# Kernel optimization log

Hardware: AMD Instinct MI355X
Metric: run time of the kernel (lower is better)

Reference implementation:

```python
import jax, jax.numpy as jnp
import numpy as np
from jax import lax

GN_GROUPS = 8
GN_EPS = 1e-5
K_BITS = 8
DELTA = 0.05
EPS = 1e-8


def setup_inputs() -> dict:
    key = jax.random.key(0)
    k1, k2 = jax.random.split(key)
    B, Cin, H, W = 32, 256, 56, 56
    Cout, KS = 256, 3
    x = jax.random.normal(k1, (B, Cin, H, W), dtype=jnp.float32)
    # kaiming_normal_(nonlinearity='relu'): std = sqrt(2 / fan_in)
    fan_in = Cin * KS * KS
    weight_fp = jax.random.normal(k2, (Cout, Cin, KS, KS), dtype=jnp.float32) * np.sqrt(2.0 / fan_in)
    gamma = jnp.ones((Cin,), dtype=jnp.float32)
    beta = jnp.zeros((Cin,), dtype=jnp.float32)
    a = jnp.asarray(6.0, dtype=jnp.float32)  # PACT learnable clip
    bias = jnp.zeros((Cout,), dtype=jnp.float32)
    return {"x": x, "gamma": gamma, "beta": beta, "a": a, "weight_fp": weight_fp, "bias": bias}


def _group_norm(x, gamma, beta):
    B, C, H, W = x.shape
    xg = x.reshape(B, GN_GROUPS, -1)
    mu = xg.mean(axis=-1, keepdims=True)
    var = xg.var(axis=-1, keepdims=True)  # biased, matches torch GroupNorm
    xn = ((xg - mu) * lax.rsqrt(var + GN_EPS)).reshape(B, C, H, W)
    return xn * gamma[:, None, None] + beta[:, None, None]


def _pact_quant(x, a):
    a_c = jnp.maximum(a, 0.0) + EPS
    S = (2.0 ** K_BITS - 1.0) / a_c
    y = jnp.clip(x, 0.0, a_c)
    # straight-through round
    return y + lax.stop_gradient(jnp.round(y * S) / S - y)


def _ternary_weight(w_r):
    oc = w_r.shape[0]
    wv = w_r.reshape(oc, -1)
    wa = jnp.abs(wv)
    t = DELTA * wa.mean(axis=1, keepdims=True)
    m = (wa > t).astype(wv.dtype)
    alpha = (wa * m).sum(axis=1, keepdims=True) / (m.sum(axis=1, keepdims=True) + EPS)
    wq = (alpha * jnp.sign(wv) * m).reshape(w_r.shape)
    # STE gradient factor: m + 0.5*(1 - m)
    g = lax.stop_gradient((0.5 + 0.5 * m).reshape(w_r.shape))
    return g * w_r + lax.stop_gradient(wq - g * w_r)


def reference(x, gamma, beta, a, weight_fp, bias):
    h = _group_norm(x, gamma, beta)
    h = jnp.maximum(h, 0.0) ** 2          # ReLU^2
    h = _pact_quant(h, a)                  # PACT k-bit uniform quant
    w = _ternary_weight(weight_fp)         # ternary {-alpha, 0, +alpha}
    out = lax.conv_general_dilated(
        h, w, window_strides=(1, 1), padding=[(1, 1), (1, 1)],
        dimension_numbers=("NCHW", "OIHW", "NCHW"))
    return out + bias[:, None, None]
```

## Files before the change

### kernel.cpp

```cpp
#include <hip/hip_runtime.h>
#include <hip/hip_bf16.h>

#define B_    32
#define C_    256
#define H_    56
#define W_    56
#define HW_   3136
#define P_    58
#define G_    8
#define COUT_ 256
#define KTOT_ 2304

typedef float f32x4 __attribute__((ext_vector_type(4)));
typedef int   i32x4 __attribute__((ext_vector_type(4)));

__global__ __launch_bounds__(1024)
void gn_stats_kernel(const float* __restrict__ x, float* __restrict__ stats) {
    int bg = blockIdx.x;
    const float4* base = (const float4*)(x + (size_t)bg * (32 * HW_));
    float s1 = 0.f, s2 = 0.f;
    for (int i = threadIdx.x; i < 25088; i += 1024) {
        float4 v = base[i];
        s1 += v.x + v.y + v.z + v.w;
        s2 += v.x * v.x + v.y * v.y + v.z * v.z + v.w * v.w;
    }
    #pragma unroll
    for (int off = 32; off; off >>= 1) {
        s1 += __shfl_down(s1, off, 64);
        s2 += __shfl_down(s2, off, 64);
    }
    __shared__ float ra[16], rb[16];
    int lane = threadIdx.x & 63, wv = threadIdx.x >> 6;
    if (!lane) { ra[wv] = s1; rb[wv] = s2; }
    __syncthreads();
    if (threadIdx.x == 0) {
        float t1 = 0.f, t2 = 0.f;
        #pragma unroll
        for (int i = 0; i < 16; ++i) { t1 += ra[i]; t2 += rb[i]; }
        float mu = t1 / 100352.f;
        float var = t2 / 100352.f - mu * mu;
        stats[bg * 2]     = mu;
        stats[bg * 2 + 1] = rsqrtf(var + 1e-5f);
    }
}

__global__ __launch_bounds__(256)
void act_kernel(const float* __restrict__ x, const float* __restrict__ gamma,
                const float* __restrict__ beta, const float* __restrict__ a_ptr,
                const float* __restrict__ stats, char* __restrict__ q) {
    int by = blockIdx.x;
    int b = by / P_;
    int y = by - b * P_;
    char* qrow = q + (size_t)by * P_ * C_;
    const int PADV = 0x80808080;
    if (y == 0 || y == P_ - 1) {
        int4 pv = {PADV, PADV, PADV, PADV};
        for (int i = threadIdx.x; i < (P_ * C_) / 16; i += 256)
            ((int4*)qrow)[i] = pv;
        return;
    }
    int t = threadIdx.x;
    if (t < 64)            ((int*)qrow)[t] = PADV;
    else if (t < 128)      ((int*)(qrow + (P_ - 1) * C_))[t - 64] = PADV;

    float a_c = fmaxf(a_ptr[0], 0.f) + 1e-8f;
    float S   = 255.f / a_c;

    int c4 = t & 63;
    int wb = t >> 6;
    int g  = (4 * c4) >> 5;
    float mu = stats[(b * G_ + g) * 2];
    float rs = stats[(b * G_ + g) * 2 + 1];
    float ga[4], be[4];
    #pragma unroll
    for (int i = 0; i < 4; ++i) { ga[i] = gamma[4 * c4 + i]; be[i] = beta[4 * c4 + i]; }

    const float* xb = x + ((size_t)(b * C_ + 4 * c4)) * HW_ + (y - 1) * W_;
    for (int j = wb; j < 14; j += 4) {
        float4 v[4];
        #pragma unroll
        for (int i = 0; i < 4; ++i)
            v[i] = *(const float4*)(xb + (size_t)i * HW_ + j * 4);
        int qv[4][4];
        #pragma unroll
        for (int i = 0; i < 4; ++i) {
            float f[4] = {v[i].x, v[i].y, v[i].z, v[i].w};
            #pragma unroll
            for (int s = 0; s < 4; ++s) {
                float yv = (f[s] - mu) * rs * ga[i] + be[i];
                float r  = fmaxf(yv, 0.f);
                float h2 = fminf(r * r, a_c);
                qv[i][s] = (int)rintf(h2 * S) - 128;
            }
        }
        #pragma unroll
        for (int s = 0; s < 4; ++s) {
            int packed = (qv[0][s] & 255) | ((qv[1][s] & 255) << 8) |
                         ((qv[2][s] & 255) << 16) | (qv[3][s] << 24);
            *(int*)(qrow + (j * 4 + s + 1) * C_ + 4 * c4) = packed;
        }
    }
}

__global__ __launch_bounds__(256)
void wq_kernel(const float* __restrict__ wfp, char* __restrict__ wt,
               float* __restrict__ alphas, float* __restrict__ tsum) {
    int oc = blockIdx.x;
    int t  = threadIdx.x;
    const float* wr = wfp + (size_t)oc * KTOT_;
    float wl[9];
    float s = 0.f;
    #pragma unroll
    for (int j = 0; j < 9; ++j) { wl[j] = wr[t + j * 256]; s += fabsf(wl[j]); }

    __shared__ float red[4];
    int lane = t & 63, wv = t >> 6;
    #pragma unroll
    for (int off = 32; off; off >>= 1) s += __shfl_down(s, off, 64);
    if (!lane) red[wv] = s;
    __syncthreads();
    float thr = 0.05f * ((red[0] + red[1] + red[2] + red[3]) / (float)KTOT_);
    __syncthreads();

    float sm = 0.f, cnt = 0.f, ts = 0.f;
    #pragma unroll
    for (int j = 0; j < 9; ++j) {
        float aw = fabsf(wl[j]);
        if (aw > thr) {
            sm += aw; cnt += 1.f;
            ts += (wl[j] > 0.f) ? 1.f : -1.f;
        }
    }
    #pragma unroll
    for (int off = 32; off; off >>= 1) {
        sm  += __shfl_down(sm, off, 64);
        cnt += __shfl_down(cnt, off, 64);
        ts  += __shfl_down(ts, off, 64);
    }
    __shared__ float redc[4], redt[4];
    if (!lane) { red[wv] = sm; redc[wv] = cnt; redt[wv] = ts; }
    __syncthreads();
    if (t == 0) {
        float alpha = (red[0] + red[1] + red[2] + red[3]) /
                      (redc[0] + redc[1] + redc[2] + redc[3] + 1e-8f);
        alphas[oc] = alpha;
        tsum[oc] = redt[0] + redt[1] + redt[2] + redt[3];
    }
    #pragma unroll
    for (int j = 0; j < 9; ++j) {
        int i  = t + j * 256;
        int ic = i / 9;
        int tap = i - ic * 9;
        float w = wl[j];
        char tern = (fabsf(w) > thr) ? (w > 0.f ? (char)1 : (char)-1) : (char)0;
        wt[((size_t)tap * 256 + oc) * 256 + ic] = tern;
    }
}

__global__ __launch_bounds__(512)
void conv_gemm_kernel(const char* __restrict__ q, const char* __restrict__ wt,
                      const float* __restrict__ alphas, const float* __restrict__ bias,
                      const float* __restrict__ tsum, const float* __restrict__ a_ptr,
                      float* __restrict__ out) {
    int mt = blockIdx.x;
    int tid = threadIdx.x;
    int lane = tid & 63;
    int wv = tid >> 6;
    int wm = wv & 1, wn = wv >> 1;
    int quad = lane >> 4, lrow = lane & 15;

    __shared__ char As[128 * 128];
    __shared__ char Bs[256 * 128];

    int kswz = (((tid & 7) ^ ((tid >> 3) & 7)) << 4);
    int sb[2], wb[4];
    #pragma unroll
    for (int r = 0; r < 2; ++r) {
        int ml = r * 64 + (tid >> 3);
        int m = mt * 128 + ml;
        int b = m / HW_;
        int rem = m - b * HW_;
        int hh = rem / W_;
        int ww = rem - hh * W_;
        sb[r] = ((b * P_ + hh + 1) * P_ + (ww + 1)) * C_ + kswz;
    }
    #pragma unroll
    for (int r = 0; r < 4; ++r) {
        int oc = r * 64 + (tid >> 3);
        wb[r] = oc * C_ + kswz;
    }

    i32x4 acc[4][4];
    #pragma unroll
    for (int i = 0; i < 4; ++i)
        #pragma unroll
        for (int j = 0; j < 4; ++j) { acc[i][j][0]=0; acc[i][j][1]=0; acc[i][j][2]=0; acc[i][j][3]=0; }

    int arow = wm * 64 + lrow;
    int brow = wn * 64 + lrow;
    int rsw = lrow & 7;

    for (int kk = 0; kk < 18; ++kk) {
        int tap = kk >> 1;
        int ic0 = (kk & 1) << 7;
        int dh = tap / 3 - 1;
        int dw = tap - (tap / 3) * 3 - 1;
        int aoff = (dh * P_ + dw) * C_ + ic0;
        const char* gb = wt + (size_t)tap * (256 * 256) + ic0;
        #pragma unroll
        for (int r = 0; r < 2; ++r) {
            __builtin_amdgcn_global_load_lds(
                (const __attribute__((address_space(1))) void*)(q + sb[r] + aoff),
                (__attribute__((address_space(3))) void*)(&As[r * 8192 + tid * 16]),
                16, 0, 0);
        }
        #pragma unroll
        for (int r = 0; r < 4; ++r) {
            __builtin_amdgcn_global_load_lds(
                (const __attribute__((address_space(1))) void*)(gb + wb[r]),
                (__attribute__((address_space(3))) void*)(&Bs[r * 8192 + tid * 16]),
                16, 0, 0);
        }
        __syncthreads();
        #pragma unroll
        for (int ks = 0; ks < 2; ++ks) {
            int cb = (ks * 4 + quad) ^ rsw;
            i32x4 af[4], bf[4];
            #pragma unroll
            for (int mi = 0; mi < 4; ++mi)
                af[mi] = *(const i32x4*)&As[(arow + mi * 16) * 128 + cb * 16];
            #pragma unroll
            for (int ni = 0; ni < 4; ++ni)
                bf[ni] = *(const i32x4*)&Bs[(brow + ni * 16) * 128 + cb * 16];
            #pragma unroll
            for (int mi = 0; mi < 4; ++mi)
                #pragma unroll
                for (int ni = 0; ni < 4; ++ni)
                    acc[mi][ni] = __builtin_amdgcn_mfma_i32_16x16x64_i8(
                        af[mi], bf[ni], acc[mi][ni], 0, 0, 0);
        }
        __syncthreads();
    }

    float a_c = fmaxf(a_ptr[0], 0.f) + 1e-8f;
    float qs  = a_c * (1.f / 255.f);
    #pragma unroll
    for (int ni = 0; ni < 4; ++ni) {
        int n = wn * 64 + ni * 16 + lrow;
        float sc = alphas[n] * qs;
        float bn = bias[n];
        float corr = 128.f * tsum[n];
        #pragma unroll
        for (int mi = 0; mi < 4; ++mi) {
            int mbase = mt * 128 + wm * 64 + mi * 16 + quad * 4;
            int b = mbase / HW_;
            size_t off = (size_t)b * (C_ * HW_) + (size_t)n * HW_ + (mbase - b * HW_);
            f32x4 v;
            #pragma unroll
            for (int r = 0; r < 4; ++r)
                v[r] = ((float)acc[mi][ni][r] + corr) * sc + bn;
            *(f32x4*)(out + off) = v;
        }
    }
}

extern "C" void kernel_launch(void* const* d_in, const int* in_sizes, int n_in,
                              void* d_out, int out_size, void* d_ws, size_t ws_size,
                              hipStream_t stream) {
    const float* x     = (const float*)d_in[0];
    const float* gamma = (const float*)d_in[1];
    const float* beta  = (const float*)d_in[2];
    const float* a     = (const float*)d_in[3];
    const float* wfp   = (const float*)d_in[4];
    const float* bias  = (const float*)d_in[5];
    float* out = (float*)d_out;

    char* ws = (char*)d_ws;
    char*  qbuf   = ws;
    char*  wtb    = ws + 27557888;
    float* alphas = (float*)(ws + 27557888 + 589824);
    float* tsum   = alphas + 256;
    float* stats  = tsum + 256;

    gn_stats_kernel<<<B_ * G_, 1024, 0, stream>>>(x, stats);
    wq_kernel<<<COUT_, 256, 0, stream>>>(wfp, wtb, alphas, tsum);
    act_kernel<<<B_ * P_, 256, 0, stream>>>(x, gamma, beta, a, stats, qbuf);
    conv_gemm_kernel<<<784, 512, 0, stream>>>(qbuf, wtb, alphas, bias, tsum, a, out);
}
```

Before: 291.2 us.

## Double-buffer LDS tiles and interleave next-tile prefetch with MFMA phases

Splits shared memory into two buffers so the next K-step's A and B tiles are loaded asynchronously into LDS while the current tile is consumed. The MFMA work is broken into four phases separated by barriers, with the global-to-LDS loads spread between them, and s_setprio raises wave priority around the MFMA bursts. The goal is to hide global load latency behind compute. In exchange, LDS use doubles to 96KB per block, which may cut occupancy, and the extra barriers add synchronisation.

```diff
diff --git a/kernel.cpp b/kernel.cpp
--- a/kernel.cpp
+++ b/kernel.cpp
@@ -169,8 +169,8 @@
     int wm = wv & 1, wn = wv >> 1;
     int quad = lane >> 4, lrow = lane & 15;
 
-    __shared__ char As[128 * 128];
-    __shared__ char Bs[256 * 128];
+    __shared__ char As[2][128 * 128];
+    __shared__ char Bs[2][256 * 128];
 
     int kswz = (((tid & 7) ^ ((tid >> 3) & 7)) << 4);
     int sb[2], wb[4];
@@ -200,46 +200,114 @@
     int brow = wn * 64 + lrow;
     int rsw = lrow & 7;
 
-    for (int kk = 0; kk < 18; ++kk) {
+    auto stageA = [&](int kk, int buf) {
         int tap = kk >> 1;
         int ic0 = (kk & 1) << 7;
         int dh = tap / 3 - 1;
         int dw = tap - (tap / 3) * 3 - 1;
         int aoff = (dh * P_ + dw) * C_ + ic0;
-        const char* gb = wt + (size_t)tap * (256 * 256) + ic0;
         #pragma unroll
         for (int r = 0; r < 2; ++r) {
             __builtin_amdgcn_global_load_lds(
                 (const __attribute__((address_space(1))) void*)(q + sb[r] + aoff),
-                (__attribute__((address_space(3))) void*)(&As[r * 8192 + tid * 16]),
+                (__attribute__((address_space(3))) void*)(&As[buf][r * 8192 + tid * 16]),
                 16, 0, 0);
         }
-        #pragma unroll
-        for (int r = 0; r < 4; ++r) {
+    };
+    auto stageB = [&](int kk, int buf, int half) {
+        int tap = kk >> 1;
+        int ic0 = (kk & 1) << 7;
+        const char* gb = wt + (size_t)tap * (256 * 256) + ic0;
+        #pragma unroll
+        for (int r = 0; r < 2; ++r) {
+            int rr = half * 2 + r;
             __builtin_amdgcn_global_load_lds(
-                (const __attribute__((address_space(1))) void*)(gb + wb[r]),
-                (__attribute__((address_space(3))) void*)(&Bs[r * 8192 + tid * 16]),
+                (const __attribute__((address_space(1))) void*)(gb + wb[rr]),
+                (__attribute__((address_space(3))) void*)(&Bs[buf][rr * 8192 + tid * 16]),
                 16, 0, 0);
         }
+    };
+
+    stageA(0, 0);
+    stageB(0, 0, 0);
+    stageB(0, 0, 1);
+    __syncthreads();
+
+    int cur = 0;
+    for (int kk = 0; kk < 18; ++kk) {
+        int nxt = cur ^ 1;
+        bool pf = (kk < 17);
+        i32x4 bf[4];
+
+        if (pf) stageA(kk + 1, nxt);
+        {
+            int cb = quad ^ rsw;
+            #pragma unroll
+            for (int ni = 0; ni < 4; ++ni)
+                bf[ni] = *(const i32x4*)&Bs[cur][(brow + ni * 16) * 128 + cb * 16];
+            i32x4 a0 = *(const i32x4*)&As[cur][(arow +  0) * 128 + cb * 16];
+            i32x4 a1 = *(const i32x4*)&As[cur][(arow + 16) * 128 + cb * 16];
+            __builtin_amdgcn_s_setprio(1);
+            #pragma unroll
+            for (int ni = 0; ni < 4; ++ni)
+                acc[0][ni] = __builtin_amdgcn_mfma_i32_16x16x64_i8(a0, bf[ni], acc[0][ni], 0, 0, 0);
+            #pragma unroll
+            for (int ni = 0; ni < 4; ++ni)
+                acc[1][ni] = __builtin_amdgcn_mfma_i32_16x16x64_i8(a1, bf[ni], acc[1][ni], 0, 0, 0);
+            __builtin_amdgcn_s_setprio(0);
+        }
+        __builtin_amdgcn_s_barrier();
+
+        if (pf) stageB(kk + 1, nxt, 0);
+        {
+            int cb = quad ^ rsw;
+            i32x4 a2 = *(const i32x4*)&As[cur][(arow + 32) * 128 + cb * 16];
+            i32x4 a3 = *(const i32x4*)&As[cur][(arow + 48) * 128 + cb * 16];
+            __builtin_amdgcn_s_setprio(1);
+            #pragma unroll
+            for (int ni = 0; ni < 4; ++ni)
+                acc[2][ni] = __builtin_amdgcn_mfma_i32_16x16x64_i8(a2, bf[ni], acc[2][ni], 0, 0, 0);
+            #pragma unroll
+            for (int ni = 0; ni < 4; ++ni)
+                acc[3][ni] = __builtin_amdgcn_mfma_i32_16x16x64_i8(a3, bf[ni], acc[3][ni], 0, 0, 0);
+            __builtin_amdgcn_s_setprio(0);
+        }
+        __builtin_amdgcn_s_barrier();
+
+        if (pf) stageB(kk + 1, nxt, 1);
+        {
+            int cb = (4 + quad) ^ rsw;
+            #pragma unroll
+            for (int ni = 0; ni < 4; ++ni)
+                bf[ni] = *(const i32x4*)&Bs[cur][(brow + ni * 16) * 128 + cb * 16];
+            i32x4 a0 = *(const i32x4*)&As[cur][(arow +  0) * 128 + cb * 16];
+            i32x4 a1 = *(const i32x4*)&As[cur][(arow + 16) * 128 + cb * 16];
+            __builtin_amdgcn_s_setprio(1);
+            #pragma unroll
+            for (int ni = 0; ni < 4; ++ni)
+                acc[0][ni] = __builtin_amdgcn_mfma_i32_16x16x64_i8(a0, bf[ni], acc[0][ni], 0, 0, 0);
+            #pragma unroll
+            for (int ni = 0; ni < 4; ++ni)
+                acc[1][ni] = __builtin_amdgcn_mfma_i32_16x16x64_i8(a1, bf[ni], acc[1][ni], 0, 0, 0);
+            __builtin_amdgcn_s_setprio(0);
+        }
+        __builtin_amdgcn_s_barrier();
+
+        {
+            int cb = (4 + quad) ^ rsw;
+            i32x4 a2 = *(const i32x4*)&As[cur][(arow + 32) * 128 + cb * 16];
+            i32x4 a3 = *(const i32x4*)&As[cur][(arow + 48) * 128 + cb * 16];
+            __builtin_amdgcn_s_setprio(1);
+            #pragma unroll
+            for (int ni = 0; ni < 4; ++ni)
+                acc[2][ni] = __builtin_amdgcn_mfma_i32_16x16x64_i8(a2, bf[ni], acc[2][ni], 0, 0, 0);
+            #pragma unroll
+            for (int ni = 0; ni < 4; ++ni)
+                acc[3][ni] = __builtin_amdgcn_mfma_i32_16x16x64_i8(a3, bf[ni], acc[3][ni], 0, 0, 0);
+            __builtin_amdgcn_s_setprio(0);
+        }
         __syncthreads();
-        #pragma unroll
-        for (int ks = 0; ks < 2; ++ks) {
-            int cb = (ks * 4 + quad) ^ rsw;
-            i32x4 af[4], bf[4];
-            #pragma unroll
-            for (int mi = 0; mi < 4; ++mi)
-                af[mi] = *(const i32x4*)&As[(arow + mi * 16) * 128 + cb * 16];
-            #pragma unroll
-            for (int ni = 0; ni < 4; ++ni)
-                bf[ni] = *(const i32x4*)&Bs[(brow + ni * 16) * 128 + cb * 16];
-            #pragma unroll
-            for (int mi = 0; mi < 4; ++mi)
-                #pragma unroll
-                for (int ni = 0; ni < 4; ++ni)
-                    acc[mi][ni] = __builtin_amdgcn_mfma_i32_16x16x64_i8(
-                        af[mi], bf[ni], acc[mi][ni], 0, 0, 0);
-        }
-        __syncthreads();
+        cur = nxt;
     }
 
     float a_c = fmaxf(a_ptr[0], 0.f) + 1e-8f;
```

Result: slower. 341.2 us (+17.2%).
